# Performance work log

Hardware: AMD Instinct MI355X
Metric: run time of the kernel (lower is better)

The kernel has to match this reference:

```python
import jax, jax.numpy as jnp
import numpy as np

TEMPERATURE = 8.0  # sqrt(d_k=64)


def setup_inputs() -> dict:
    key = jax.random.key(0)
    kq, kk, kv, km = jax.random.split(key, 4)
    B, S, D = 16, 2048, 64
    q = jax.random.normal(kq, (B, S, D), dtype=jnp.float32)
    k = jax.random.normal(kk, (B, S, D), dtype=jnp.float32)
    v = jax.random.normal(kv, (B, S, D), dtype=jnp.float32)
    mask = jax.random.randint(km, (1, S, S), 0, 2, dtype=jnp.int32)
    return {"q": q, "k": k, "v": v, "mask": mask}


def reference(q, k, v, mask):
    # scores: [B, S, S] = (q / temperature) @ k^T
    attn = jnp.einsum('bsd,btd->bst', q / TEMPERATURE, k)
    attn = jnp.where(mask == 0, jnp.float32(-1e9), attn)
    attn = jax.nn.softmax(attn, axis=-1)
    # dropout is identity in eval-mode math (source stores float, not a module)
    output = jnp.einsum('bst,btd->bsd', attn, v)
    return (output, attn)
```

## Files before the change

### kernel.cpp

```cpp
#include <hip/hip_runtime.h>

constexpr int NB = 16;
constexpr int NS = 2048;
constexpr int ND = 64;
constexpr int MTILE = 16;
constexpr int NW32 = NS / 32;

typedef __attribute__((ext_vector_type(8))) short bh8;
typedef __attribute__((ext_vector_type(4))) float f32x4;
typedef __attribute__((ext_vector_type(4))) unsigned short us4;

constexpr int EB_STRIDE = 2048 + 8;

__device__ __forceinline__ unsigned short f2bf(float x) {
  unsigned u = __float_as_uint(x);
  u += 0x7fffu + ((u >> 16) & 1u);
  return (unsigned short)(u >> 16);
}
__device__ __forceinline__ float bf2f(unsigned u16) {
  return __uint_as_float(u16 << 16);
}

__global__ __launch_bounds__(256)
void prep_kv_kernel(const float* __restrict__ v, const float* __restrict__ k,
                    unsigned short* __restrict__ vt, unsigned short* __restrict__ kbf) {
  __shared__ float tile[64][65];
  const int b   = blockIdx.y;
  const int kc  = blockIdx.x;
  const int tid = threadIdx.x;
  const int r0  = tid >> 4;
  const int c0  = (tid & 15) * 4;
  #pragma unroll
  for (int p = 0; p < 4; ++p) {
    const int krow = p * 16 + r0;
    const long base = ((long)(b * NS) + kc * 64 + krow) * ND + c0;
    float4 vv = *(const float4*)(v + base);
    tile[c0 + 0][krow] = vv.x;
    tile[c0 + 1][krow] = vv.y;
    tile[c0 + 2][krow] = vv.z;
    tile[c0 + 3][krow] = vv.w;
    float4 kk4 = *(const float4*)(k + base);
    us4 ko;
    ko.x = f2bf(kk4.x); ko.y = f2bf(kk4.y); ko.z = f2bf(kk4.z); ko.w = f2bf(kk4.w);
    *(us4*)(kbf + base) = ko;
  }
  __syncthreads();
  #pragma unroll
  for (int p = 0; p < 4; ++p) {
    const int d = p * 16 + r0;
    us4 o;
    o.x = f2bf(tile[d][c0 + 0]);
    o.y = f2bf(tile[d][c0 + 1]);
    o.z = f2bf(tile[d][c0 + 2]);
    o.w = f2bf(tile[d][c0 + 3]);
    *(us4*)(vt + ((long)(b * 64 + d)) * NS + kc * 64 + c0) = o;
  }
}

__global__ __launch_bounds__(256)
void maskpack_kernel(const int* __restrict__ mask, unsigned* __restrict__ mbits) {
  const int row = blockIdx.y;
  const int col = blockIdx.x * 256 + threadIdx.x;
  const unsigned long long bal = __ballot(mask[(long)row * NS + col] != 0);
  const int lane = threadIdx.x & 63;
  if (lane == 0)       mbits[row * NW32 + (col >> 5)] = (unsigned)bal;
  else if (lane == 32) mbits[row * NW32 + (col >> 5)] = (unsigned)(bal >> 32);
}

__global__ __launch_bounds__(512, 1)
void sdpa_fused_kernel(const float* __restrict__ q, const unsigned short* __restrict__ kbf,
                       const unsigned* __restrict__ mbits, const unsigned short* __restrict__ vt,
                       float* __restrict__ outO, float* __restrict__ outA)
{
  extern __shared__ char smem[];
  unsigned short* ebuf = (unsigned short*)smem;
  float* rowsumP = (float*)(ebuf + MTILE * EB_STRIDE);
  float* invl    = rowsumP + 16 * 8;
  float* osum    = invl + 16;

  const int tid  = threadIdx.x;
  const int wave = tid >> 6;
  const int lane = tid & 63;
  const int n16  = lane & 15;
  const int quad = lane >> 4;
  const int b     = blockIdx.y;
  const int mbase = blockIdx.x * MTILE;

  const int col0 = wave * 256;
  const int r0q  = quad * 4;

  bh8 aq[2];
  {
    const float* qp = q + ((long)(b * NS + mbase + n16)) * ND + quad * 8;
    #pragma unroll
    for (int kk = 0; kk < 2; ++kk) {
      float4 x0 = *(const float4*)(qp + kk * 32);
      float4 x1 = *(const float4*)(qp + kk * 32 + 4);
      bh8 f;
      f[0] = f2bf(x0.x * 0.125f); f[1] = f2bf(x0.y * 0.125f);
      f[2] = f2bf(x0.z * 0.125f); f[3] = f2bf(x0.w * 0.125f);
      f[4] = f2bf(x1.x * 0.125f); f[5] = f2bf(x1.y * 0.125f);
      f[6] = f2bf(x1.z * 0.125f); f[7] = f2bf(x1.w * 0.125f);
      aq[kk] = f;
    }
  }

  const unsigned short* kbp = kbf + (long)(b * NS) * ND;
  float rsum[4] = {0.f, 0.f, 0.f, 0.f};
  #pragma unroll 2
  for (int nt2 = 0; nt2 < 8; ++nt2) {
    unsigned mrow[4];
    #pragma unroll
    for (int r = 0; r < 4; ++r)
      mrow[r] = mbits[(long)(mbase + r0q + r) * NW32 + (col0 >> 5) + nt2];
    #pragma unroll
    for (int half = 0; half < 2; ++half) {
      const int key = col0 + nt2 * 32 + half * 16 + n16;
      const unsigned short* kp = kbp + (long)key * ND + quad * 8;
      bh8 f0 = *(const bh8*)(kp);
      bh8 f1 = *(const bh8*)(kp + 32);
      f32x4 acc = {0.f, 0.f, 0.f, 0.f};
      acc = __builtin_amdgcn_mfma_f32_16x16x32_bf16(aq[0], f0, acc, 0, 0, 0);
      acc = __builtin_amdgcn_mfma_f32_16x16x32_bf16(aq[1], f1, acc, 0, 0, 0);
      #pragma unroll
      for (int r = 0; r < 4; ++r) {
        const unsigned bit = (mrow[r] >> (half * 16 + n16)) & 1u;
        const float e = bit ? __expf(acc[r]) : 0.f;
        rsum[r] += e;
        ebuf[(r0q + r) * EB_STRIDE + key] = f2bf(e);
      }
    }
  }

  #pragma unroll
  for (int r = 0; r < 4; ++r) {
    float s = rsum[r];
    s += __shfl_xor(s, 1);
    s += __shfl_xor(s, 2);
    s += __shfl_xor(s, 4);
    s += __shfl_xor(s, 8);
    if (n16 == 0) rowsumP[(r0q + r) * 8 + wave] = s;
  }
  __syncthreads();
  if (tid < 16) {
    float l = 0.f;
    #pragma unroll
    for (int c = 0; c < 8; ++c) l += rowsumP[tid * 8 + c];
    invl[tid] = 1.f / l;
  }
  __syncthreads();

  {
    float* aout = outA + ((long)(b * NS + mbase)) * NS;
    const int c4 = tid * 4;
    #pragma unroll 2
    for (int row = 0; row < MTILE; ++row) {
      const float il = invl[row];
      uint2 raw = *(const uint2*)(ebuf + row * EB_STRIDE + c4);
      float4 o;
      o.x = bf2f(raw.x & 0xffffu) * il;
      o.y = bf2f(raw.x >> 16)     * il;
      o.z = bf2f(raw.y & 0xffffu) * il;
      o.w = bf2f(raw.y >> 16)     * il;
      *(float4*)(aout + (long)row * NS + c4) = o;
    }
  }

  const int dtile = wave & 3;
  const int khalf = wave >> 2;
  const int kbase = khalf * 1024;
  const unsigned short* vrow = vt + ((long)(b * 64 + dtile * 16 + n16)) * NS + kbase + quad * 8;
  f32x4 oacc = {0.f, 0.f, 0.f, 0.f};
  #pragma unroll 4
  for (int kc = 0; kc < 32; ++kc) {
    const int k0 = kbase + kc * 32;
    bh8 af = *(const bh8*)(ebuf + n16 * EB_STRIDE + k0 + quad * 8);
    bh8 bf = *(const bh8*)(vrow + kc * 32);
    oacc = __builtin_amdgcn_mfma_f32_16x16x32_bf16(af, bf, oacc, 0, 0, 0);
  }
  if (khalf == 1) *(f32x4*)(osum + (dtile * 64 + lane) * 4) = oacc;
  __syncthreads();
  if (khalf == 0) {
    f32x4 other = *(const f32x4*)(osum + (dtile * 64 + lane) * 4);
    #pragma unroll
    for (int r = 0; r < 4; ++r) {
      const int lrow = quad * 4 + r;
      outO[((long)(b * NS + mbase + lrow)) * ND + dtile * 16 + n16] =
          (oacc[r] + other[r]) * invl[lrow];
    }
  }
}

extern "C" void kernel_launch(void* const* d_in, const int* in_sizes, int n_in,
                              void* d_out, int out_size, void* d_ws, size_t ws_size,
                              hipStream_t stream) {
  const float* q    = (const float*)d_in[0];
  const float* k    = (const float*)d_in[1];
  const float* v    = (const float*)d_in[2];
  const int*   mask = (const int*)d_in[3];
  float* outO = (float*)d_out;
  float* outA = outO + (long)NB * NS * ND;

  unsigned short* vt    = (unsigned short*)d_ws;
  unsigned short* kbf   = vt + (long)NB * ND * NS;
  unsigned*       mbits = (unsigned*)(kbf + (long)NB * NS * ND);

  prep_kv_kernel<<<dim3(NS / 64, NB), 256, 0, stream>>>(v, k, vt, kbf);
  maskpack_kernel<<<dim3(NS / 256, NS), 256, 0, stream>>>(mask, mbits);

  const size_t lds = (size_t)(MTILE * EB_STRIDE) * sizeof(short)
                   + (size_t)(16 * 8 + 16 + 4 * 64 * 4) * sizeof(float);
  hipFuncSetAttribute((const void*)sdpa_fused_kernel,
                      hipFuncAttributeMaxDynamicSharedMemorySize, (int)lds);
  sdpa_fused_kernel<<<dim3(NS / MTILE, NB), 512, lds, stream>>>(q, kbf, mbits, vt, outO, outA);
}
```

Baseline: 460.2 us.

## Swizzle block order, double-buffer K loads, and interleave attn stores with PV MFMA

Remaps block indices so that consecutive blocks spread across batches, intended to balance L2/XCD use. Software-pipelines the QK^T loop by double-buffering K fragments and mask words two groups ahead. It also interleaves the normalized attention-row writeback with the PV MFMA loop so memory stores overlap compute, and uses nontemporal stores for both outputs. The costs are higher register pressure and more complex code, and the swizzle hardcodes the grid shape.

```diff
diff --git a/kernel.cpp b/kernel.cpp
--- a/kernel.cpp
+++ b/kernel.cpp
@@ -83,8 +83,11 @@
   const int lane = tid & 63;
   const int n16  = lane & 15;
   const int quad = lane >> 4;
-  const int b     = blockIdx.y;
-  const int mbase = blockIdx.x * MTILE;
+
+  const int bid   = blockIdx.y * gridDim.x + blockIdx.x;
+  const int swz   = (bid & 7) * 256 + (bid >> 3);
+  const int b     = swz >> 7;
+  const int mbase = (swz & 127) * MTILE;
 
   const int col0 = wave * 256;
   const int r0q  = quad * 4;
@@ -105,32 +108,53 @@
     }
   }
 
-  const unsigned short* kbp = kbf + (long)(b * NS) * ND;
+  const unsigned short* kbp = kbf + (long)(b * NS) * ND + quad * 8;
   float rsum[4] = {0.f, 0.f, 0.f, 0.f};
-  #pragma unroll 2
-  for (int nt2 = 0; nt2 < 8; ++nt2) {
-    unsigned mrow[4];
-    #pragma unroll
-    for (int r = 0; r < 4; ++r)
-      mrow[r] = mbits[(long)(mbase + r0q + r) * NW32 + (col0 >> 5) + nt2];
-    #pragma unroll
-    for (int half = 0; half < 2; ++half) {
-      const int key = col0 + nt2 * 32 + half * 16 + n16;
-      const unsigned short* kp = kbp + (long)key * ND + quad * 8;
-      bh8 f0 = *(const bh8*)(kp);
-      bh8 f1 = *(const bh8*)(kp + 32);
-      f32x4 acc = {0.f, 0.f, 0.f, 0.f};
-      acc = __builtin_amdgcn_mfma_f32_16x16x32_bf16(aq[0], f0, acc, 0, 0, 0);
-      acc = __builtin_amdgcn_mfma_f32_16x16x32_bf16(aq[1], f1, acc, 0, 0, 0);
-      #pragma unroll
-      for (int r = 0; r < 4; ++r) {
-        const unsigned bit = (mrow[r] >> (half * 16 + n16)) & 1u;
-        const float e = bit ? __expf(acc[r]) : 0.f;
-        rsum[r] += e;
-        ebuf[(r0q + r) * EB_STRIDE + key] = f2bf(e);
-      }
-    }
-  }
+
+#define LOADG(kf, mw, g) do {                                                   \
+    const int kk0 = col0 + (g) * 32;                                            \
+    const unsigned short* kp = kbp + (long)(kk0 + n16) * ND;                    \
+    kf[0] = *(const bh8*)(kp);                                                  \
+    kf[1] = *(const bh8*)(kp + 32);                                             \
+    kf[2] = *(const bh8*)(kp + 16 * ND);                                        \
+    kf[3] = *(const bh8*)(kp + 16 * ND + 32);                                   \
+    _Pragma("unroll")                                                           \
+    for (int r = 0; r < 4; ++r)                                                 \
+      mw[r] = mbits[(long)(mbase + r0q + r) * NW32 + (kk0 >> 5)];               \
+  } while (0)
+
+#define COMPUTEG(kf, mw, g) do {                                                \
+    _Pragma("unroll")                                                           \
+    for (int h = 0; h < 2; ++h) {                                               \
+      f32x4 acc = {0.f, 0.f, 0.f, 0.f};                                         \
+      acc = __builtin_amdgcn_mfma_f32_16x16x32_bf16(aq[0], kf[2*h],   acc,0,0,0);\
+      acc = __builtin_amdgcn_mfma_f32_16x16x32_bf16(aq[1], kf[2*h+1], acc,0,0,0);\
+      const int key = col0 + (g) * 32 + h * 16 + n16;                           \
+      _Pragma("unroll")                                                         \
+      for (int r = 0; r < 4; ++r) {                                             \
+        const unsigned bit = (mw[r] >> (h * 16 + n16)) & 1u;                    \
+        const float e = bit ? __expf(acc[r]) : 0.f;                             \
+        rsum[r] += e;                                                           \
+        ebuf[(r0q + r) * EB_STRIDE + key] = f2bf(e);                            \
+      }                                                                         \
+    }                                                                           \
+  } while (0)
+
+  {
+    bh8 kfA[4], kfB[4];
+    unsigned mwA[4], mwB[4];
+    LOADG(kfA, mwA, 0); LOADG(kfB, mwB, 1);
+    COMPUTEG(kfA, mwA, 0); LOADG(kfA, mwA, 2);
+    COMPUTEG(kfB, mwB, 1); LOADG(kfB, mwB, 3);
+    COMPUTEG(kfA, mwA, 2); LOADG(kfA, mwA, 4);
+    COMPUTEG(kfB, mwB, 3); LOADG(kfB, mwB, 5);
+    COMPUTEG(kfA, mwA, 4); LOADG(kfA, mwA, 6);
+    COMPUTEG(kfB, mwB, 5); LOADG(kfB, mwB, 7);
+    COMPUTEG(kfA, mwA, 6);
+    COMPUTEG(kfB, mwB, 7);
+  }
+#undef LOADG
+#undef COMPUTEG
 
   #pragma unroll
   for (int r = 0; r < 4; ++r) {
@@ -150,33 +174,30 @@
   }
   __syncthreads();
 
-  {
-    float* aout = outA + ((long)(b * NS + mbase)) * NS;
-    const int c4 = tid * 4;
-    #pragma unroll 2
-    for (int row = 0; row < MTILE; ++row) {
+  const int dtile = wave & 3;
+  const int khalf = wave >> 2;
+  const int kb    = khalf * 1024;
+  const unsigned short* vrow = vt + ((long)(b * 64 + dtile * 16 + n16)) * NS + kb + quad * 8;
+  float* aout = outA + ((long)(b * NS + mbase)) * NS;
+  const int c4 = tid * 4;
+  f32x4 oacc = {0.f, 0.f, 0.f, 0.f};
+  #pragma unroll 8
+  for (int kc = 0; kc < 32; ++kc) {
+    const int k0 = kb + kc * 32;
+    bh8 af  = *(const bh8*)(ebuf + n16 * EB_STRIDE + k0 + quad * 8);
+    bh8 bfv = *(const bh8*)(vrow + kc * 32);
+    oacc = __builtin_amdgcn_mfma_f32_16x16x32_bf16(af, bfv, oacc, 0, 0, 0);
+    if (kc & 1) {
+      const int row = kc >> 1;
       const float il = invl[row];
       uint2 raw = *(const uint2*)(ebuf + row * EB_STRIDE + c4);
-      float4 o;
-      o.x = bf2f(raw.x & 0xffffu) * il;
-      o.y = bf2f(raw.x >> 16)     * il;
-      o.z = bf2f(raw.y & 0xffffu) * il;
-      o.w = bf2f(raw.y >> 16)     * il;
-      *(float4*)(aout + (long)row * NS + c4) = o;
+      f32x4 o;
+      o[0] = bf2f(raw.x & 0xffffu) * il;
+      o[1] = bf2f(raw.x >> 16)     * il;
+      o[2] = bf2f(raw.y & 0xffffu) * il;
+      o[3] = bf2f(raw.y >> 16)     * il;
+      __builtin_nontemporal_store(o, (f32x4*)(aout + (long)row * NS + c4));
     }
-  }
-
-  const int dtile = wave & 3;
-  const int khalf = wave >> 2;
-  const int kbase = khalf * 1024;
-  const unsigned short* vrow = vt + ((long)(b * 64 + dtile * 16 + n16)) * NS + kbase + quad * 8;
-  f32x4 oacc = {0.f, 0.f, 0.f, 0.f};
-  #pragma unroll 4
-  for (int kc = 0; kc < 32; ++kc) {
-    const int k0 = kbase + kc * 32;
-    bh8 af = *(const bh8*)(ebuf + n16 * EB_STRIDE + k0 + quad * 8);
-    bh8 bf = *(const bh8*)(vrow + kc * 32);
-    oacc = __builtin_amdgcn_mfma_f32_16x16x32_bf16(af, bf, oacc, 0, 0, 0);
   }
   if (khalf == 1) *(f32x4*)(osum + (dtile * 64 + lane) * 4) = oacc;
   __syncthreads();
@@ -185,8 +206,9 @@
     #pragma unroll
     for (int r = 0; r < 4; ++r) {
       const int lrow = quad * 4 + r;
-      outO[((long)(b * NS + mbase + lrow)) * ND + dtile * 16 + n16] =
-          (oacc[r] + other[r]) * invl[lrow];
+      __builtin_nontemporal_store(
+          (oacc[r] + other[r]) * invl[lrow],
+          outO + ((long)(b * NS + mbase + lrow)) * ND + dtile * 16 + n16);
     }
   }
 }
```

New measurement: 400.3 us. 1.15x faster.
